# Kernel tuning notes

Measured on AMD Instinct MI355X. Metric: run time of the kernel, lower is better.

## Reference

```python
import jax, jax.numpy as jnp
import numpy as np

D_MODEL, KAN_HIDDEN, NUM, K = 1024, 128, 3, 3  # grid_size=3, spline order k=3
GRID_RANGE = (-1.0, 1.0)


def make_grid(in_dim):
    # extended grid: num+1 interior knots padded by k steps of h on each side -> num+1+2k points
    h = (GRID_RANGE[1] - GRID_RANGE[0]) / NUM
    g = jnp.arange(-K, NUM + K + 1, dtype=jnp.float32) * h + GRID_RANGE[0]  # [num+1+2k]
    return jnp.broadcast_to(g, (in_dim, g.shape[0]))  # [in_dim, G]


def b_splines(x, grid):
    # Cox-de-Boor recursion. x: [N, D], grid: [D, G] -> basis [N, D, G-1-K]
    xg = x[:, :, None]  # [N, D, 1]
    B = ((xg >= grid[None, :, :-1]) & (xg < grid[None, :, 1:])).astype(x.dtype)
    for d in range(1, K + 1):
        left = (xg - grid[None, :, : -(d + 1)]) / (grid[:, d:-1] - grid[:, : -(d + 1)])[None]
        right = (grid[None, :, d + 1:] - xg) / (grid[:, d + 1:] - grid[:, 1:-d])[None]
        B = left * B[:, :, :-1] + right * B[:, :, 1:]
    return B  # [N, D, NUM+K]


def kan_layer(x, grid, coef, scale_base, scale_sp):
    # y[n,i,o] = scale_base[i,o]*silu(x[n,i]) + scale_sp[i,o]*sum_g B[n,i,g]*coef[i,o,g]; out = y.sum(i)
    B = b_splines(x, grid)  # [N, in, NUM+K]
    spline = jnp.einsum('nig,iog->no', B, coef * scale_sp[:, :, None])
    base = jnp.einsum('ni,io->no', jax.nn.silu(x), scale_base)
    return base + spline  # [N, out]


def setup_inputs() -> dict:
    key = jax.random.key(0)
    ks = jax.random.split(key, 7)
    s = 0.1  # small init scale for spline coefficients, matching noisy init spirit
    return {
        'x': jax.random.normal(ks[0], (4, 4096, D_MODEL), dtype=jnp.float32),
        'coef1': jax.random.normal(ks[1], (D_MODEL, KAN_HIDDEN, NUM + K), dtype=jnp.float32) * s,
        'scale_base1': jax.random.normal(ks[2], (D_MODEL, KAN_HIDDEN), dtype=jnp.float32),
        'scale_sp1': jnp.ones((D_MODEL, KAN_HIDDEN), dtype=jnp.float32),
        'coef2': jax.random.normal(ks[3], (KAN_HIDDEN, D_MODEL, NUM + K), dtype=jnp.float32) * s,
        'scale_base2': jax.random.normal(ks[4], (KAN_HIDDEN, D_MODEL), dtype=jnp.float32),
        'scale_sp2': jnp.ones((KAN_HIDDEN, D_MODEL), dtype=jnp.float32),
    }


def reference(x, coef1, scale_base1, scale_sp1, coef2, scale_base2, scale_sp2):
    b, s, d = x.shape
    xf = x.reshape(-1, d)  # [N, d_model]
    g1 = make_grid(D_MODEL)
    g2 = make_grid(KAN_HIDDEN)
    y1 = kan_layer(xf, g1, coef1, scale_base1, scale_sp1)   # [N, kan_hidden]
    y2 = kan_layer(y1, g2, coef2, scale_base2, scale_sp2)   # [N, d_model]
    return y2.reshape(b, s, d)
```

## Files before the change

kernel.cpp:

```cpp
#include <hip/hip_runtime.h>
#include <stdint.h>

typedef float f32x4 __attribute__((ext_vector_type(4)));
typedef __bf16 bf16x8 __attribute__((ext_vector_type(8)));
typedef __bf16 bf16x2 __attribute__((ext_vector_type(2)));
typedef unsigned short ushort4v __attribute__((ext_vector_type(4)));

#define NROW 16384
#define DM   1024
#define HID  128
#define K1   8192
#define K2   1024
#define KSPLIT 4

__device__ __forceinline__ unsigned short f2bf(float f) {
  unsigned u = __builtin_bit_cast(unsigned, f);
  u += 0x7fffu + ((u >> 16) & 1u);
  return (unsigned short)(u >> 16);
}

__device__ __forceinline__ uint32_t pk2(float lo, float hi) {
  bf16x2 v;
  v[0] = (__bf16)lo;
  v[1] = (__bf16)hi;
  return __builtin_bit_cast(uint32_t, v);
}

__device__ __forceinline__ void g2l16(const void* g, void* l) {
  __builtin_amdgcn_global_load_lds(
      (const __attribute__((address_space(1))) unsigned int*)g,
      (__attribute__((address_space(3))) unsigned int*)l, 16, 0, 0);
}

__device__ __forceinline__ bf16x8 expand8(float v) {
  const float t = (v + 3.0f) * 1.5f;
  const float cf = floorf(t);
  const float u = t - cf;
  int c = (int)cf;
  c = c < -1 ? -1 : c;
  c = c > 9 ? 9 : c;
  const float u2 = u * u, u3 = u2 * u, omu = 1.0f - u;
  const float p0 = u3 * (1.0f / 6.0f);
  float p1 = __builtin_fmaf(0.5f, u, 1.0f / 6.0f);
  p1 = __builtin_fmaf(0.5f, u2, p1);
  p1 = __builtin_fmaf(-0.5f, u3, p1);
  float p2 = __builtin_fmaf(0.5f, u3, 4.0f / 6.0f);
  p2 = p2 - u2;
  const float p3 = (omu * omu) * (omu * (1.0f / 6.0f));
  const uint64_t W = (uint64_t)pk2(p3, p2) | ((uint64_t)pk2(p1, p0) << 32);
  const int sa = (c - 2) * 16;
  const int sl = sa & 63;
  const uint64_t t1 = W << sl;
  const uint64_t t2 = (W >> (63 - sl)) >> 1;
  const uint64_t t3 = W >> ((-sa) & 63);
  const uint64_t L = sa < 0 ? t3 : (sa < 64 ? t1 : 0);
  const uint64_t H = sa < 0 ? 0  : (sa < 64 ? t2 : t1);
  const float e = __expf(-v);
  const float s = v * __builtin_amdgcn_rcpf(1.0f + e);
  const uint32_t su = __builtin_bit_cast(uint32_t, s);
  const uint32_t shf_bits = su & 0xffff0000u;
  const float slo_f = s - __builtin_bit_cast(float, shf_bits);
  const uint32_t slo = (uint32_t)__builtin_bit_cast(unsigned short, (__bf16)slo_f);
  const uint32_t w0 = ((uint32_t)L & 0xffff0000u) | (shf_bits >> 16);
  const uint32_t w1 = (uint32_t)(L >> 32);
  const uint32_t w2 = (uint32_t)H;
  const uint32_t w3 = ((uint32_t)(H >> 32) & 0xffffu) | (slo << 16);
  union { uint4 q; bf16x8 b; } r;
  r.q = (uint4){w0, w1, w2, w3};
  return r.b;
}

__global__ void kan_prep_w1(const float* __restrict__ c1, const float* __restrict__ sb1,
                            const float* __restrict__ sp1, unsigned short* __restrict__ w1t) {
  const int t = blockIdx.x * 256 + threadIdx.x;
  const int o = t >> 10, i = t & 1023;
  const float sb = sb1[i * HID + o], sp = sp1[i * HID + o];
  const float* cf = c1 + (size_t)(i * HID + o) * 6;
  union { uint4 u; unsigned short h[8]; } r;
  const unsigned short b = f2bf(sb);
  r.h[0] = b; r.h[7] = b;
#pragma unroll
  for (int g = 0; g < 6; ++g) r.h[g + 1] = f2bf(cf[g] * sp);
  *(uint4*)(w1t + (size_t)o * K1 + i * 8) = r.u;
}

__global__ void kan_prep_w2(const float* __restrict__ c2, const float* __restrict__ sb2,
                            const float* __restrict__ sp2, unsigned short* __restrict__ w2t) {
  const int t = blockIdx.x * 256 + threadIdx.x;
  const int o = t >> 7, i = t & 127;
  const float sb = sb2[i * DM + o], sp = sp2[i * DM + o];
  const float* cf = c2 + (size_t)(i * DM + o) * 6;
  union { uint4 u; unsigned short h[8]; } r;
  const unsigned short b = f2bf(sb);
  r.h[0] = b; r.h[7] = b;
#pragma unroll
  for (int g = 0; g < 6; ++g) r.h[g + 1] = f2bf(cf[g] * sp);
  *(uint4*)(w2t + (size_t)o * K2 + i * 8) = r.u;
}

__global__ __launch_bounds__(512, 4) void kan_gemm1(
    const float* __restrict__ x, const unsigned short* __restrict__ w1t,
    unsigned short* __restrict__ yq) {
  __shared__ __align__(16) char lds[32768];
  const int tid = threadIdx.x;
  const int lane = tid & 63, w = tid >> 6;
  const int wk = w >> 2, wm = (w >> 1) & 1, wn = w & 1;
  const int mt = blockIdx.x >> 2, kh = blockIdx.x & 3;
  const int m0 = mt * 128;
  const int arow = tid >> 2, acs = (tid & 3) * 2;

  f32x4 acc[4][4];
#pragma unroll
  for (int a = 0; a < 4; ++a)
#pragma unroll
    for (int b = 0; b < 4; ++b) acc[a][b] = (f32x4){0.f, 0.f, 0.f, 0.f};

  const int bo = wn * 64 + (lane & 15);
  const unsigned short* bp = w1t + (size_t)bo * K1 + kh * 2048 + wk * 32 + (lane >> 4) * 8;

  const int wraw = arow * 128 + acs * 16;
  const int wsw = (arow & 7) << 4;
  char* wa0 = lds + (wraw ^ wsw);
  char* wa1 = lds + ((wraw + 16) ^ wsw);
  const char* ra[4];
#pragma unroll
  for (int mi = 0; mi < 4; ++mi) {
    const int row = wm * 64 + mi * 16 + (lane & 15);
    ra[mi] = lds + ((row * 128 + wk * 64 + (lane >> 4) * 16) ^ ((row & 7) << 4));
  }
  const float* xrow = x + (size_t)(m0 + arow) * DM + kh * 256 + acs;

  bf16x8 b[4], af[4];
  const int NT = 32;

  {
    float2 xv0 = *(const float2*)xrow;
    *(bf16x8*)wa0 = expand8(xv0.x);
    *(bf16x8*)wa1 = expand8(xv0.y);
  }
  float2 xv = *(const float2*)(xrow + 8);
  __syncthreads();

  for (int kt = 0; kt < NT; ++kt) {
    const int cur = kt & 1;
#pragma unroll
    for (int ni = 0; ni < 4; ++ni)
      b[ni] = *(const bf16x8*)(bp + (size_t)ni * 16 * K1 + kt * 64);
    if (kt + 1 < NT) {
      const int nb = (cur ^ 1) * 16384;
      *(bf16x8*)(wa0 + nb) = expand8(xv.x);
      *(bf16x8*)(wa1 + nb) = expand8(xv.y);
      xv = *(const float2*)(xrow + ((kt + 2 < NT) ? kt + 2 : NT - 1) * 8);
    }
#pragma unroll
    for (int mi = 0; mi < 4; ++mi)
      af[mi] = *(const bf16x8*)(ra[mi] + cur * 16384);
#pragma unroll
    for (int mi = 0; mi < 4; ++mi)
#pragma unroll
      for (int ni = 0; ni < 4; ++ni)
        acc[mi][ni] = __builtin_amdgcn_mfma_f32_16x16x32_bf16(af[mi], b[ni], acc[mi][ni], 0, 0, 0);
    __syncthreads();
  }

  unsigned short* yb = yq + (size_t)kh * NROW * HID;
#pragma unroll
  for (int rnd = 0; rnd < 2; ++rnd) {
    const int src0 = 4 + rnd * 2;
    if (w == src0 || w == src0 + 1) {
      char* r = lds + (w - src0) * 16384;
#pragma unroll
      for (int mi = 0; mi < 4; ++mi)
#pragma unroll
        for (int ni = 0; ni < 4; ++ni)
          *(f32x4*)(r + (mi * 4 + ni) * 1024 + lane * 16) = acc[mi][ni];
    }
    __syncthreads();
    const int snk0 = rnd * 2;
    if (w == snk0 || w == snk0 + 1) {
      const char* r = lds + (w - snk0) * 16384;
#pragma unroll
      for (int mi = 0; mi < 4; ++mi)
#pragma unroll
        for (int ni = 0; ni < 4; ++ni) {
          f32x4 o = *(const f32x4*)(r + (mi * 4 + ni) * 1024 + lane * 16);
          o += acc[mi][ni];
          const int col = wn * 64 + ni * 16 + (lane & 15);
#pragma unroll
          for (int rr = 0; rr < 4; ++rr) {
            const int row = wm * 64 + mi * 16 + (lane >> 4) * 4 + rr;
            yb[(size_t)(m0 + row) * HID + col] = __builtin_bit_cast(unsigned short, (__bf16)o[rr]);
          }
        }
    }
    __syncthreads();
  }
}

__global__ void kan_combine(const unsigned short* __restrict__ yq, unsigned short* __restrict__ a2) {
  const size_t i4 = ((size_t)blockIdx.x * 256 + threadIdx.x) * 4;
  float v[4] = {0.f, 0.f, 0.f, 0.f};
#pragma unroll
  for (int h = 0; h < KSPLIT; ++h) {
    ushort4v q = *(const ushort4v*)(yq + (size_t)h * NROW * HID + i4);
#pragma unroll
    for (int j = 0; j < 4; ++j)
      v[j] += __builtin_bit_cast(float, (uint32_t)q[j] << 16);
  }
#pragma unroll
  for (int j = 0; j < 4; ++j)
    *(bf16x8*)(a2 + (i4 + j) * 8) = expand8(v[j]);
}

__global__ __launch_bounds__(256, 2) void kan_gemm2(
    const unsigned short* __restrict__ a2, const unsigned short* __restrict__ w2t,
    float* __restrict__ out) {
  __shared__ __align__(16) unsigned short lds[2 * 16384];
  const int tid = threadIdx.x;
  const int lane = tid & 63, w = tid >> 6;
  const int wm = w >> 1, wn = w & 1;
  const int mt = blockIdx.x & 127, nt = blockIdx.x >> 7;
  const int m0 = mt * 128, n0 = nt * 128;

  f32x4 acc[4][4];
#pragma unroll
  for (int a = 0; a < 4; ++a)
#pragma unroll
    for (int b = 0; b < 4; ++b) acc[a][b] = (f32x4){0.f, 0.f, 0.f, 0.f};

  auto stage = [&](int kt, int buf) {
#pragma unroll
    for (int q = 0; q < 4; ++q) {
      const int r = (w * 4 + q) * 8 + (lane >> 3);
      const int slot = (lane & 7) ^ (lane >> 3);
      g2l16(a2 + (size_t)(m0 + r) * K2 + kt * 64 + slot * 8,
            (char*)lds + buf * 32768 + (w * 4 + q) * 1024);
      g2l16(w2t + (size_t)(n0 + r) * K2 + kt * 64 + slot * 8,
            (char*)lds + buf * 32768 + 16384 + (w * 4 + q) * 1024);
    }
  };

  stage(0, 0);
  for (int kt = 0; kt < 16; ++kt) {
    const int cur = kt & 1;
    if (kt + 1 < 16) {
      stage(kt + 1, cur ^ 1);
      asm volatile("s_waitcnt vmcnt(8)" ::: "memory");
    } else {
      asm volatile("s_waitcnt vmcnt(0)" ::: "memory");
    }
    __builtin_amdgcn_sched_barrier(0);
    __builtin_amdgcn_s_barrier();
    const char* ab = (const char*)lds + cur * 32768;
    const char* bb = ab + 16384;
#pragma unroll
    for (int ks = 0; ks < 2; ++ks) {
      bf16x8 af[4], bfr[4];
#pragma unroll
      for (int mi = 0; mi < 4; ++mi) {
        const int row = wm * 64 + mi * 16 + (lane & 15);
        af[mi] = *(const bf16x8*)(ab + ((row * 128 + ks * 64 + (lane >> 4) * 16) ^ ((row & 7) << 4)));
      }
#pragma unroll
      for (int ni = 0; ni < 4; ++ni) {
        const int col = wn * 64 + ni * 16 + (lane & 15);
        bfr[ni] = *(const bf16x8*)(bb + ((col * 128 + ks * 64 + (lane >> 4) * 16) ^ ((col & 7) << 4)));
      }
#pragma unroll
      for (int mi = 0; mi < 4; ++mi)
#pragma unroll
        for (int ni = 0; ni < 4; ++ni)
          acc[mi][ni] = __builtin_amdgcn_mfma_f32_16x16x32_bf16(af[mi], bfr[ni], acc[mi][ni], 0, 0, 0);
    }
    __builtin_amdgcn_s_barrier();
  }

#pragma unroll
  for (int mi = 0; mi < 4; ++mi)
#pragma unroll
    for (int r = 0; r < 4; ++r) {
      const int row = wm * 64 + mi * 16 + (lane >> 4) * 4 + r;
#pragma unroll
      for (int ni = 0; ni < 4; ++ni) {
        const int col = wn * 64 + ni * 16 + (lane & 15);
        out[(size_t)(m0 + row) * DM + n0 + col] = acc[mi][ni][r];
      }
    }
}

extern "C" void kernel_launch(void* const* d_in, const int* in_sizes, int n_in,
                              void* d_out, int out_size, void* d_ws, size_t ws_size,
                              hipStream_t stream) {
  const float* x   = (const float*)d_in[0];
  const float* c1  = (const float*)d_in[1];
  const float* sb1 = (const float*)d_in[2];
  const float* sp1 = (const float*)d_in[3];
  const float* c2  = (const float*)d_in[4];
  const float* sb2 = (const float*)d_in[5];
  const float* sp2 = (const float*)d_in[6];
  float* out = (float*)d_out;

  unsigned short* w1t = (unsigned short*)d_ws;
  unsigned short* w2t = w1t + (size_t)HID * K1;
  unsigned short* a2  = w2t + (size_t)DM * K2;
  unsigned short* yq  = a2 + (size_t)NROW * K2;

  kan_prep_w1<<<512, 256, 0, stream>>>(c1, sb1, sp1, w1t);
  kan_prep_w2<<<512, 256, 0, stream>>>(c2, sb2, sp2, w2t);
  kan_gemm1<<<512, 512, 0, stream>>>(x, w1t, yq);
  kan_combine<<<NROW * HID / 1024, 256, 0, stream>>>(yq, a2);
  kan_gemm2<<<(NROW / 128) * (DM / 128), 256, 0, stream>>>(a2, w2t, out);
}
```

Measured before the change: 135.7 us.

## Load GEMM1 A operand directly into registers and widen per-wave N tile

Rewrites the first GEMM so each wave loads its x values straight from global memory and expands them to bf16 operand fragments in registers. This removes the LDS staging buffer and the per-iteration block barrier. Blocks shrink from 8 to 4 waves, and each wave now covers all 128 output columns (8 N tiles) with a 2-way K split reduced through LDS at the end. The cost is twice the accumulator registers per wave, fewer resident waves, and uncoalesced scalar x loads repeated across lanes.

```diff
diff --git a/kernel.cpp b/kernel.cpp
--- a/kernel.cpp
+++ b/kernel.cpp
@@ -98,102 +98,80 @@
   *(uint4*)(w2t + (size_t)o * K2 + i * 8) = r.u;
 }
 
-__global__ __launch_bounds__(512, 4) void kan_gemm1(
+__global__ __launch_bounds__(256, 2) void kan_gemm1(
     const float* __restrict__ x, const unsigned short* __restrict__ w1t,
     unsigned short* __restrict__ yq) {
-  __shared__ __align__(16) char lds[32768];
+  __shared__ __align__(16) char lds[65536];
   const int tid = threadIdx.x;
   const int lane = tid & 63, w = tid >> 6;
-  const int wk = w >> 2, wm = (w >> 1) & 1, wn = w & 1;
+  const int wm = w >> 1, wk = w & 1;
   const int mt = blockIdx.x >> 2, kh = blockIdx.x & 3;
   const int m0 = mt * 128;
-  const int arow = tid >> 2, acs = (tid & 3) * 2;
-
-  f32x4 acc[4][4];
+
+  f32x4 acc[4][8];
 #pragma unroll
   for (int a = 0; a < 4; ++a)
 #pragma unroll
-    for (int b = 0; b < 4; ++b) acc[a][b] = (f32x4){0.f, 0.f, 0.f, 0.f};
-
-  const int bo = wn * 64 + (lane & 15);
-  const unsigned short* bp = w1t + (size_t)bo * K1 + kh * 2048 + wk * 32 + (lane >> 4) * 8;
-
-  const int wraw = arow * 128 + acs * 16;
-  const int wsw = (arow & 7) << 4;
-  char* wa0 = lds + (wraw ^ wsw);
-  char* wa1 = lds + ((wraw + 16) ^ wsw);
-  const char* ra[4];
-#pragma unroll
-  for (int mi = 0; mi < 4; ++mi) {
-    const int row = wm * 64 + mi * 16 + (lane & 15);
-    ra[mi] = lds + ((row * 128 + wk * 64 + (lane >> 4) * 16) ^ ((row & 7) << 4));
-  }
-  const float* xrow = x + (size_t)(m0 + arow) * DM + kh * 256 + acs;
-
-  bf16x8 b[4], af[4];
+    for (int b = 0; b < 8; ++b) acc[a][b] = (f32x4){0.f, 0.f, 0.f, 0.f};
+
+  const int arow = m0 + wm * 64 + (lane & 15);
+  const float* xp[4];
+#pragma unroll
+  for (int mi = 0; mi < 4; ++mi)
+    xp[mi] = x + (size_t)(arow + mi * 16) * DM + kh * 256 + wk * 4 + (lane >> 4);
+
+  const unsigned short* bp =
+      w1t + (size_t)(lane & 15) * K1 + kh * 2048 + wk * 32 + (lane >> 4) * 8;
+
   const int NT = 32;
-
-  {
-    float2 xv0 = *(const float2*)xrow;
-    *(bf16x8*)wa0 = expand8(xv0.x);
-    *(bf16x8*)wa1 = expand8(xv0.y);
-  }
-  float2 xv = *(const float2*)(xrow + 8);
+  float xc[4], xn[4];
+#pragma unroll
+  for (int mi = 0; mi < 4; ++mi) xc[mi] = xp[mi][0];
+
+  for (int kt = 0; kt < NT; ++kt) {
+    bf16x8 b[8], af[4];
+#pragma unroll
+    for (int ni = 0; ni < 8; ++ni)
+      b[ni] = *(const bf16x8*)(bp + (size_t)ni * 16 * K1 + kt * 64);
+    const int nk = (kt + 1 < NT) ? kt + 1 : NT - 1;
+#pragma unroll
+    for (int mi = 0; mi < 4; ++mi) xn[mi] = xp[mi][nk * 8];
+#pragma unroll
+    for (int mi = 0; mi < 4; ++mi) af[mi] = expand8(xc[mi]);
+#pragma unroll
+    for (int mi = 0; mi < 4; ++mi)
+#pragma unroll
+      for (int ni = 0; ni < 8; ++ni)
+        acc[mi][ni] = __builtin_amdgcn_mfma_f32_16x16x32_bf16(af[mi], b[ni], acc[mi][ni], 0, 0, 0);
+#pragma unroll
+    for (int mi = 0; mi < 4; ++mi) xc[mi] = xn[mi];
+  }
+
+  if (wk == 1) {
+    char* r = lds + wm * 32768;
+#pragma unroll
+    for (int mi = 0; mi < 4; ++mi)
+#pragma unroll
+      for (int ni = 0; ni < 8; ++ni)
+        *(f32x4*)(r + (mi * 8 + ni) * 1024 + lane * 16) = acc[mi][ni];
+  }
   __syncthreads();
-
-  for (int kt = 0; kt < NT; ++kt) {
-    const int cur = kt & 1;
-#pragma unroll
-    for (int ni = 0; ni < 4; ++ni)
-      b[ni] = *(const bf16x8*)(bp + (size_t)ni * 16 * K1 + kt * 64);
-    if (kt + 1 < NT) {
-      const int nb = (cur ^ 1) * 16384;
-      *(bf16x8*)(wa0 + nb) = expand8(xv.x);
-      *(bf16x8*)(wa1 + nb) = expand8(xv.y);
-      xv = *(const float2*)(xrow + ((kt + 2 < NT) ? kt + 2 : NT - 1) * 8);
-    }
+  if (wk == 0) {
+    const char* r = lds + wm * 32768;
+    unsigned short* yb = yq + (size_t)kh * NROW * HID;
 #pragma unroll
     for (int mi = 0; mi < 4; ++mi)
-      af[mi] = *(const bf16x8*)(ra[mi] + cur * 16384);
-#pragma unroll
-    for (int mi = 0; mi < 4; ++mi)
-#pragma unroll
-      for (int ni = 0; ni < 4; ++ni)
-        acc[mi][ni] = __builtin_amdgcn_mfma_f32_16x16x32_bf16(af[mi], b[ni], acc[mi][ni], 0, 0, 0);
-    __syncthreads();
-  }
-
-  unsigned short* yb = yq + (size_t)kh * NROW * HID;
-#pragma unroll
-  for (int rnd = 0; rnd < 2; ++rnd) {
-    const int src0 = 4 + rnd * 2;
-    if (w == src0 || w == src0 + 1) {
-      char* r = lds + (w - src0) * 16384;
-#pragma unroll
-      for (int mi = 0; mi < 4; ++mi)
-#pragma unroll
-        for (int ni = 0; ni < 4; ++ni)
-          *(f32x4*)(r + (mi * 4 + ni) * 1024 + lane * 16) = acc[mi][ni];
-    }
-    __syncthreads();
-    const int snk0 = rnd * 2;
-    if (w == snk0 || w == snk0 + 1) {
-      const char* r = lds + (w - snk0) * 16384;
-#pragma unroll
-      for (int mi = 0; mi < 4; ++mi)
-#pragma unroll
-        for (int ni = 0; ni < 4; ++ni) {
-          f32x4 o = *(const f32x4*)(r + (mi * 4 + ni) * 1024 + lane * 16);
-          o += acc[mi][ni];
-          const int col = wn * 64 + ni * 16 + (lane & 15);
-#pragma unroll
-          for (int rr = 0; rr < 4; ++rr) {
-            const int row = wm * 64 + mi * 16 + (lane >> 4) * 4 + rr;
-            yb[(size_t)(m0 + row) * HID + col] = __builtin_bit_cast(unsigned short, (__bf16)o[rr]);
-          }
+#pragma unroll
+      for (int ni = 0; ni < 8; ++ni) {
+        f32x4 o = *(const f32x4*)(r + (mi * 8 + ni) * 1024 + lane * 16);
+        o += acc[mi][ni];
+        const int col = ni * 16 + (lane & 15);
+#pragma unroll
+        for (int rr = 0; rr < 4; ++rr) {
+          const int row = wm * 64 + mi * 16 + (lane >> 4) * 4 + rr;
+          yb[(size_t)(m0 + row) * HID + col] = __builtin_bit_cast(unsigned short, (__bf16)o[rr]);
         }
-    }
-    __syncthreads();
+      }
   }
 }
 
@@ -307,7 +285,7 @@
 
   kan_prep_w1<<<512, 256, 0, stream>>>(c1, sb1, sp1, w1t);
   kan_prep_w2<<<512, 256, 0, stream>>>(c2, sb2, sp2, w2t);
-  kan_gemm1<<<512, 512, 0, stream>>>(x, w1t, yq);
+  kan_gemm1<<<512, 256, 0, stream>>>(x, w1t, yq);
   kan_combine<<<NROW * HID / 1024, 256, 0, stream>>>(yq, a2);
   kan_gemm2<<<(NROW / 128) * (DM / 128), 256, 0, stream>>>(a2, w2t, out);
 }
```

New measurement: 157.5 us. 16.0% more time.
